# Kernel tuning notes

Hardware: AMD Instinct MI355X
Metric: run time of the kernel (lower is better)

Reference implementation:

```python
import jax, jax.numpy as jnp
import numpy as np

EPS = 1e-5        # torch BatchNorm2d default eps
G = 8             # DCNv4 groups
KP = 9            # 3x3 kernel points


def conv2d(x, w):
    return jax.lax.conv_general_dilated(
        x, w, window_strides=(1, 1), padding='SAME',
        dimension_numbers=('NCHW', 'OIHW', 'NCHW'))


def bn_eval(x, g_, b_, m_, v_):
    s = g_ / jnp.sqrt(v_ + EPS)
    return x * s[None, :, None, None] + (b_ - m_ * s)[None, :, None, None]


def silu(x):
    return x * jax.nn.sigmoid(x)


def dcnv4_core(value, offset, mask):
    # value: (N,H,W,G,Cg)  offset: (N,H,W,G,K,2) (x,y)  mask: (N,H,W,G,K) unnormalized (DCNv4: no softmax)
    N, H, W, Gn, Cg = value.shape
    r = jnp.arange(-1, 2, dtype=value.dtype)              # dilation=1, pad=1, 3x3 grid
    gy, gx = jnp.meshgrid(r, r, indexing='ij')
    grid_x = gx.ravel()  # (9,)
    grid_y = gy.ravel()
    px = jnp.arange(W, dtype=value.dtype)[None, None, :, None, None] + grid_x + offset[..., 0]
    py = jnp.arange(H, dtype=value.dtype)[None, :, None, None, None] + grid_y + offset[..., 1]
    x0 = jnp.floor(px); y0 = jnp.floor(py)
    lx = px - x0; ly = py - y0
    x0i = x0.astype(jnp.int32); y0i = y0.astype(jnp.int32)
    bidx = jnp.arange(N)[:, None, None, None, None]
    gidx = jnp.arange(Gn)[None, None, None, :, None]

    def tap(yi, xi, wgt):
        valid = (yi >= 0) & (yi < H) & (xi >= 0) & (xi < W)   # zero padding outside
        v = value[bidx, jnp.clip(yi, 0, H - 1), jnp.clip(xi, 0, W - 1), gidx]  # (N,H,W,G,K,Cg)
        return v * (wgt * valid)[..., None]

    s = (tap(y0i, x0i, (1 - ly) * (1 - lx))
         + tap(y0i, x0i + 1, (1 - ly) * lx)
         + tap(y0i + 1, x0i, ly * (1 - lx))
         + tap(y0i + 1, x0i + 1, ly * lx))
    return jnp.einsum('nhwgkc,nhwgk->nhwgc', s, mask)


def dcnv4(x, val_w, val_b, om_w, om_b, outp_w, outp_b):
    # x: NCHW. DCNv4 wrapper: flatten to tokens, value_proj, offset_mask linear on raw tokens,
    # deformable aggregation, output_proj, back to NCHW.
    N, C, H, W = x.shape
    t = x.transpose(0, 2, 3, 1).reshape(N, H * W, C)
    value = (t @ val_w.T + val_b).reshape(N, H, W, G, C // G)
    om = (t @ om_w.T + om_b).reshape(N, H, W, G, KP * 3)  # per group: 2K offsets then K masks
    offset = om[..., :2 * KP].reshape(N, H, W, G, KP, 2)
    mask = om[..., 2 * KP:]
    out = dcnv4_core(value, offset, mask).reshape(N, H * W, C)
    out = out @ outp_w.T + outp_b
    return out.reshape(N, H, W, C).transpose(0, 3, 1, 2)


def setup_inputs() -> dict:
    key = jax.random.key(0)
    ks = jax.random.split(key, 32)
    W_SC = 0.05
    d = {}
    d['x'] = jax.random.normal(ks[0], (4, 256, 64, 64), jnp.float32)
    d['cv1_w'] = jax.random.normal(ks[1], (128, 256, 3, 3), jnp.float32) * W_SC
    d['cv1_bn_g'] = jax.random.uniform(ks[2], (128,), jnp.float32, 0.5, 1.5)
    d['cv1_bn_b'] = jax.random.normal(ks[3], (128,), jnp.float32) * 0.1
    d['cv1_bn_m'] = jax.random.normal(ks[4], (128,), jnp.float32) * 0.1
    d['cv1_bn_v'] = jax.random.uniform(ks[5], (128,), jnp.float32, 0.5, 1.5)
    d['cv2_w'] = jax.random.normal(ks[6], (256, 128, 3, 3), jnp.float32) * W_SC
    d['cv2_bn_g'] = jax.random.uniform(ks[7], (256,), jnp.float32, 0.5, 1.5)
    d['cv2_bn_b'] = jax.random.normal(ks[8], (256,), jnp.float32) * 0.1
    d['cv2_bn_m'] = jax.random.normal(ks[9], (256,), jnp.float32) * 0.1
    d['cv2_bn_v'] = jax.random.uniform(ks[10], (256,), jnp.float32, 0.5, 1.5)
    d['val_w'] = jax.random.normal(ks[11], (256, 256), jnp.float32) * W_SC
    d['val_b'] = jax.random.normal(ks[12], (256,), jnp.float32) * 0.01
    d['om_w'] = jax.random.normal(ks[13], (216, 256), jnp.float32) * 0.02
    d['om_b'] = jax.random.normal(ks[14], (216,), jnp.float32) * 0.01
    d['outp_w'] = jax.random.normal(ks[15], (256, 256), jnp.float32) * W_SC
    d['outp_b'] = jax.random.normal(ks[16], (256,), jnp.float32) * 0.01
    d['bn3_g'] = jax.random.uniform(ks[17], (256,), jnp.float32, 0.5, 1.5)
    d['bn3_b'] = jax.random.normal(ks[18], (256,), jnp.float32) * 0.1
    d['bn3_m'] = jax.random.normal(ks[19], (256,), jnp.float32) * 0.1
    d['bn3_v'] = jax.random.uniform(ks[20], (256,), jnp.float32, 0.5, 1.5)
    d['pw1_w'] = jax.random.normal(ks[21], (768, 256, 1, 1), jnp.float32) * W_SC
    d['pw1_b'] = jax.random.normal(ks[22], (768,), jnp.float32) * 0.01
    d['pw2_w'] = jax.random.normal(ks[23], (256, 768, 1, 1), jnp.float32) * W_SC
    d['pw2_b'] = jax.random.normal(ks[24], (256,), jnp.float32) * 0.01
    return d


def reference(x, cv1_w, cv1_bn_g, cv1_bn_b, cv1_bn_m, cv1_bn_v,
              cv2_w, cv2_bn_g, cv2_bn_b, cv2_bn_m, cv2_bn_v,
              val_w, val_b, om_w, om_b, outp_w, outp_b,
              bn3_g, bn3_b, bn3_m, bn3_v, pw1_w, pw1_b, pw2_w, pw2_b):
    # cv2(cv1(x)) branch: Conv = Conv2d(no bias) + BN + SiLU
    y = silu(bn_eval(conv2d(x, cv1_w), cv1_bn_g, cv1_bn_b, cv1_bn_m, cv1_bn_v))
    y = silu(bn_eval(conv2d(y, cv2_w), cv2_bn_g, cv2_bn_b, cv2_bn_m, cv2_bn_v))
    # dcn branch: DCNv4 -> BN -> 1x1 conv (+SiLU) -> 1x1 conv
    d = dcnv4(x, val_w, val_b, om_w, om_b, outp_w, outp_b)
    d = bn_eval(d, bn3_g, bn3_b, bn3_m, bn3_v)
    d = silu(conv2d(d, pw1_w) + pw1_b[None, :, None, None])
    d = conv2d(d, pw2_w) + pw2_b[None, :, None, None]
    return x + y + d
```

## Files before the change

### kernel.cpp

```cpp
#include <hip/hip_runtime.h>
#include <math.h>

typedef __attribute__((ext_vector_type(8))) __bf16 bf16x8;
typedef __attribute__((ext_vector_type(8))) unsigned short us8;
typedef __attribute__((ext_vector_type(4))) unsigned short us4;
typedef __attribute__((ext_vector_type(4))) float f32x4;
typedef __attribute__((ext_vector_type(4))) int i32x4;
typedef unsigned int uint32;

#define EPSV 1e-5f

__device__ __forceinline__ float silu_f(float v) { return v / (1.f + __expf(-v)); }

__device__ __forceinline__ unsigned short f2bf(float f) {
  uint32 u = __builtin_bit_cast(uint32, f);
  u += 0x7fffu + ((u >> 16) & 1u);
  return (unsigned short)(u >> 16);
}
__device__ __forceinline__ float bf2f(unsigned short h) {
  uint32 u = ((uint32)h) << 16;
  return __builtin_bit_cast(float, u);
}

__device__ __forceinline__ void gl_lds16(const void* g, void* l) {
  __builtin_amdgcn_global_load_lds(
      (const __attribute__((address_space(1))) unsigned int*)g,
      (__attribute__((address_space(3))) unsigned int*)l, 16, 0, 0);
}

template <int EPI, int CIN, int BN>
__device__ __forceinline__ void gemm_body(
    int rb, int cb, int k0, int KL,
    const unsigned short* __restrict__ A, const unsigned short* __restrict__ Bw,
    const float* __restrict__ bias, int K, int Co, void* __restrict__ outv,
    const float* __restrict__ e0, const float* __restrict__ e1,
    const float* __restrict__ e2, const float* __restrict__ e3,
    const unsigned short* __restrict__ zpage, bf16x8* smem) {
  constexpr int NFR = BN / 32;
  constexpr int NB = BN / 64;
  constexpr int CPB = 512 + BN * 4;
  const int t = threadIdx.x;
  const int lane = t & 63;
  const int wv = t >> 6;
  const int wr = wv >> 1, wc = wv & 1;

  f32x4 acc[4][NFR];
#pragma unroll
  for (int i = 0; i < 4; i++)
#pragma unroll
    for (int j = 0; j < NFR; j++) acc[i][j] = (f32x4){0.f, 0.f, 0.f, 0.f};

  const unsigned short* Abase[2];
  int aprow[2], apcol[2], akoff[2];
#pragma unroll
  for (int i = 0; i < 2; i++) {
    int c = t + 256 * i;
    int row = (c >> 6) * 16 + (c & 15);
    int koff = ((c >> 4) & 3) * 8;
    akoff[i] = koff;
    int grow = rb + row;
    if constexpr (CIN > 0) {
      int n = grow >> 12, p = grow & 4095;
      aprow[i] = p >> 6;
      apcol[i] = p & 63;
      Abase[i] = A + (size_t)n * 4096 * CIN;
    } else {
      Abase[i] = A + (size_t)grow * K + koff;
    }
  }
  const unsigned short* Bbase[NB];
#pragma unroll
  for (int i = 0; i < NB; i++) {
    int c = t + 256 * i;
    int col = cb + (c >> 6) * 16 + (c & 15);
    int koff = ((c >> 4) & 3) * 8;
    Bbase[i] = (col < Co) ? (Bw + (size_t)col * K + koff) : zpage;
  }
  auto addrA = [&](int i, int kb) -> const unsigned short* {
    if constexpr (CIN > 0) {
      int tap = kb / CIN;
      int ci = (kb & (CIN - 1)) + akoff[i];
      int dy = tap / 3 - 1, dx = tap % 3 - 1;
      int h = aprow[i] + dy, w = apcol[i] + dx;
      if (((unsigned)h < 64u) & ((unsigned)w < 64u))
        return &Abase[i][(size_t)(h * 64 + w) * CIN + ci];
      return zpage;
    } else {
      return Abase[i] + kb;
    }
  };
  auto stage = [&](int buf, int kb) {
    bf16x8* base = &smem[buf * CPB];
    gl_lds16(addrA(0, kb), (void*)&base[t]);
    gl_lds16(addrA(1, kb), (void*)&base[t + 256]);
    gl_lds16((Bbase[0] == zpage) ? zpage : Bbase[0] + kb, (void*)&base[512 + t]);
    if constexpr (NB == 2)
      gl_lds16((Bbase[1] == zpage) ? zpage : Bbase[1] + kb,
               (void*)&base[512 + t + 256]);
  };

  const int nt = KL >> 5;
  stage(0, k0);
  __syncthreads();
  int cur = 0;
  for (int it = 0; it < nt; ++it) {
    if (it + 1 < nt) stage(cur ^ 1, k0 + ((it + 1) << 5));
    const bf16x8* Ab = &smem[cur * CPB];
    const bf16x8* Bb = Ab + 512;
    bf16x8 af[4], bfr[NFR];
#pragma unroll
    for (int mi = 0; mi < 4; mi++) af[mi] = Ab[(wr * 4 + mi) * 64 + lane];
#pragma unroll
    for (int ni = 0; ni < NFR; ni++) bfr[ni] = Bb[(wc * NFR + ni) * 64 + lane];
    __builtin_amdgcn_s_setprio(1);
#pragma unroll
    for (int mi = 0; mi < 4; mi++)
#pragma unroll
      for (int ni = 0; ni < NFR; ni++)
        acc[mi][ni] = __builtin_amdgcn_mfma_f32_16x16x32_bf16(af[mi], bfr[ni],
                                                              acc[mi][ni], 0, 0, 0);
    __builtin_amdgcn_s_setprio(0);
    __syncthreads();
    cur ^= 1;
  }

  const int lr = lane & 15, kg4 = (lane >> 4) * 4;
#pragma unroll
  for (int mi = 0; mi < 4; mi++) {
#pragma unroll
    for (int ni = 0; ni < NFR; ni++) {
      int gcol = cb + wc * (BN / 2) + ni * 16 + lr;
      if (gcol >= Co) continue;
      float bval, s = 1.f, tt = 0.f;
      if (EPI == 2 || EPI == 7) bval = 0.f;
      else if (EPI == 5) bval = (gcol < 256) ? bias[gcol] : e0[gcol - 256];
      else bval = bias[gcol];
      if (EPI == 2 || EPI == 3) {
        s = e0[gcol] * rsqrtf(e3[gcol] + EPSV);
        tt = e1[gcol] - e2[gcol] * s;
      }
      if (EPI == 6) {
        int grow0 = rb + wr * 64 + mi * 16 + kg4;
        int n = grow0 >> 12, p0 = grow0 & 4095;
        size_t oix = ((size_t)(n * 256 + gcol)) * 4096 + p0;
        f32x4 xv = *(const f32x4*)&((const float*)e0)[oix];
        const unsigned short* y2p = (const unsigned short*)e1;
        f32x4 ov;
#pragma unroll
        for (int j = 0; j < 4; j++) {
          float y2 = bf2f(y2p[((size_t)(n * 4096 + p0 + j)) * 256 + gcol]);
          ov[j] = acc[mi][ni][j] + bval + xv[j] + y2;
        }
        *(f32x4*)&((float*)outv)[oix] = ov;
        continue;
      }
#pragma unroll
      for (int j = 0; j < 4; j++) {
        int grow = rb + wr * 64 + mi * 16 + kg4 + j;
        float v = acc[mi][ni][j] + bval;
        if (EPI == 2) v = silu_f(v * s + tt);
        if (EPI == 3) v = v * s + tt;
        if (EPI == 4) v = silu_f(v);
        if (EPI == 7) {
          ((float*)outv)[(size_t)grow * Co + gcol] = v;
        } else if (EPI == 5) {
          if (gcol < 256)
            ((unsigned short*)outv)[(size_t)grow * 256 + gcol] = f2bf(v);
          else
            ((float*)e1)[(size_t)grow * 216 + (gcol - 256)] = v;
        } else {
          ((unsigned short*)outv)[(size_t)grow * Co + gcol] = f2bf(v);
        }
      }
    }
  }
}

__device__ __forceinline__ void dcn_body(
    int bid, const unsigned short* __restrict__ value,
    const float* __restrict__ om, unsigned short* __restrict__ out,
    void* smemraw) {
  f32x4* wgt = (f32x4*)smemraw;
  i32x4* adr = (i32x4*)((char*)smemraw + 288 * 16);
  const int n = bid >> 10;
  const int p0 = (bid & 1023) * 4;
  const int t = threadIdx.x;

  for (int idx = t; idx < 288; idx += 256) {
    int pi = idx / 72;
    int gk = idx - pi * 72;
    int g = gk / 9, k = gk - g * 9;
    int p = p0 + pi;
    int h0 = p >> 6, w0 = p & 63;
    const float* omp = om + ((size_t)(n * 4096 + p)) * 216 + g * 27;
    float ox = omp[2 * k], oy = omp[2 * k + 1], mk = omp[18 + k];
    float px = (float)(w0 + (k % 3) - 1) + ox;
    float py = (float)(h0 + (k / 3) - 1) + oy;
    float x0f = floorf(px), y0f = floorf(py);
    float lx = px - x0f, ly = py - y0f;
    int x0 = (int)x0f, y0 = (int)y0f;
    int x1 = x0 + 1, y1 = y0 + 1;
    bool vx0 = (unsigned)x0 < 64u, vx1 = (unsigned)x1 < 64u;
    bool vy0 = (unsigned)y0 < 64u, vy1 = (unsigned)y1 < 64u;
    int cx0 = min(max(x0, 0), 63), cx1 = min(max(x1, 0), 63);
    int cy0 = min(max(y0, 0), 63), cy1 = min(max(y1, 0), 63);
    f32x4 w4;
    w4[0] = (1.f - ly) * (1.f - lx) * mk * (float)(vy0 && vx0);
    w4[1] = (1.f - ly) * lx * mk * (float)(vy0 && vx1);
    w4[2] = ly * (1.f - lx) * mk * (float)(vy1 && vx0);
    w4[3] = ly * lx * mk * (float)(vy1 && vx1);
    i32x4 a4;
    a4[0] = (cy0 * 64 + cx0) * 256;
    a4[1] = (cy0 * 64 + cx1) * 256;
    a4[2] = (cy1 * 64 + cx0) * 256;
    a4[3] = (cy1 * 64 + cx1) * 256;
    wgt[idx] = w4;
    adr[idx] = a4;
  }
  __syncthreads();

  const int pi = t >> 6;
  const int g = (t >> 3) & 7;
  const int l = t & 7;
  const int p = p0 + pi;
  const unsigned short* vb = value + ((size_t)n * 4096) * 256 + g * 32 + l * 4;
  const int bix = (pi * 8 + g) * 9;
  float a0 = 0.f, a1 = 0.f, a2 = 0.f, a3 = 0.f;
#pragma unroll
  for (int k = 0; k < 9; k++) {
    f32x4 wv = wgt[bix + k];
    i32x4 av = adr[bix + k];
    us4 q0 = *(const us4*)(vb + av[0]);
    us4 q1 = *(const us4*)(vb + av[1]);
    us4 q2 = *(const us4*)(vb + av[2]);
    us4 q3 = *(const us4*)(vb + av[3]);
    a0 += wv[0] * bf2f(q0[0]) + wv[1] * bf2f(q1[0]) + wv[2] * bf2f(q2[0]) + wv[3] * bf2f(q3[0]);
    a1 += wv[0] * bf2f(q0[1]) + wv[1] * bf2f(q1[1]) + wv[2] * bf2f(q2[1]) + wv[3] * bf2f(q3[1]);
    a2 += wv[0] * bf2f(q0[2]) + wv[1] * bf2f(q1[2]) + wv[2] * bf2f(q2[2]) + wv[3] * bf2f(q3[2]);
    a3 += wv[0] * bf2f(q0[3]) + wv[1] * bf2f(q1[3]) + wv[2] * bf2f(q2[3]) + wv[3] * bf2f(q3[3]);
  }
  us4 o;
  o[0] = f2bf(a0); o[1] = f2bf(a1); o[2] = f2bf(a2); o[3] = f2bf(a3);
  *(us4*)&out[((size_t)(n * 4096 + p)) * 256 + g * 32 + l * 4] = o;
}

__global__ __launch_bounds__(256) void prep_k(
    const float* __restrict__ x, unsigned short* __restrict__ xt,
    const float* __restrict__ c1, unsigned short* __restrict__ o1,
    const float* __restrict__ c2, unsigned short* __restrict__ o2,
    const float* __restrict__ a0, unsigned short* __restrict__ b0,
    const float* __restrict__ a1, unsigned short* __restrict__ b1,
    const float* __restrict__ a2, unsigned short* __restrict__ b2,
    const float* __restrict__ a3, unsigned short* __restrict__ b3,
    const float* __restrict__ a4, unsigned short* __restrict__ b4,
    uint32* __restrict__ zp) {
  __shared__ float lds[64][65];
  int b = blockIdx.x;
  const int t = threadIdx.x;
  if (b == 0 && t < 32) zp[t] = 0u;
  if (b < 1024) {
    const int p0 = (b & 63) * 64, c0 = ((b >> 6) & 3) * 64, n = b >> 8;
    const int pp = t & 63, ccb = t >> 6;
    const float* xb = x + ((size_t)n * 256 + c0) * 4096 + p0;
#pragma unroll
    for (int i = 0; i < 16; i++) {
      int cc = ccb * 16 + i;
      lds[pp][cc] = xb[(size_t)cc * 4096 + pp];
    }
    __syncthreads();
#pragma unroll
    for (int i = 0; i < 2; i++) {
      int pp2 = (t >> 3) + i * 32;
      int c8 = (t & 7) * 8;
      us8 v;
#pragma unroll
      for (int j = 0; j < 8; j++) v[j] = f2bf(lds[pp2][c8 + j]);
      *(us8*)&xt[((size_t)(n * 4096 + p0 + pp2)) * 256 + c0 + c8] = v;
    }
    return;
  }
  int idx = (b - 1024) * 256 + t;
  if (idx < 294912) {
    int ci = idx & 255, r = idx >> 8;
    int tap = r % 9, co = r / 9;
    o1[idx] = f2bf(c1[((size_t)co * 256 + ci) * 9 + tap]);
    return;
  }
  idx -= 294912;
  if (idx < 294912) {
    int ci = idx & 127, r = idx >> 7;
    int tap = r % 9, co = r / 9;
    o2[idx] = f2bf(c2[((size_t)co * 128 + ci) * 9 + tap]);
    return;
  }
  idx -= 294912;
  const float* s;
  unsigned short* d;
  int off;
  if (idx < 65536)       { s = a0; d = b0; off = idx; }
  else if (idx < 120832) { s = a1; d = b1; off = idx - 65536; }
  else if (idx < 186368) { s = a2; d = b2; off = idx - 120832; }
  else if (idx < 382976) { s = a3; d = b3; off = idx - 186368; }
  else if (idx < 579584) { s = a4; d = b4; off = idx - 382976; }
  else return;
  d[off] = f2bf(s[off]);
}

__global__ __launch_bounds__(256) void fused_s1(
    const unsigned short* __restrict__ xt,
    const unsigned short* __restrict__ wc1, float* __restrict__ part,
    const unsigned short* __restrict__ wval, const float* __restrict__ val_b,
    const float* __restrict__ om_b, float* __restrict__ omf,
    unsigned short* __restrict__ valt, const unsigned short* __restrict__ zpage) {
  __shared__ bf16x8 smem[2048];
  int b = blockIdx.x;
  if (b < 512) {
    int s = b >> 7, mt = b & 127;
    gemm_body<7, 256, 128>(mt * 128, 0, s * 576, 576, xt, wc1, nullptr, 2304,
                           128, part + (size_t)s * 2097152, nullptr, nullptr,
                           nullptr, nullptr, zpage, smem);
  } else {
    b -= 512;
    gemm_body<5, 0, 128>((b >> 2) * 128, (b & 3) * 128, 0, 256, xt, wval, val_b,
                         256, 472, valt, om_b, (const float*)omf, nullptr,
                         nullptr, zpage, smem);
  }
}

__global__ __launch_bounds__(256) void fused_r(
    const float* __restrict__ part, const float* __restrict__ g1,
    const float* __restrict__ bb1, const float* __restrict__ m1,
    const float* __restrict__ v1, unsigned short* __restrict__ y1t,
    const unsigned short* __restrict__ valt, const float* __restrict__ omf,
    unsigned short* __restrict__ dcnt) {
  __shared__ char rsm[9216];
  int b = blockIdx.x;
  if (b < 1024) {
    int idx = b * 256 + threadIdx.x;
    int grow = idx >> 4;
    int co8 = (idx & 15) * 8;
    size_t base = (size_t)grow * 128 + co8;
    f32x4 s0 = *(const f32x4*)&part[base];
    f32x4 s1 = *(const f32x4*)&part[base + 4];
#pragma unroll
    for (int s = 1; s < 4; s++) {
      s0 += *(const f32x4*)&part[base + (size_t)s * 2097152];
      s1 += *(const f32x4*)&part[base + (size_t)s * 2097152 + 4];
    }
    us8 o;
#pragma unroll
    for (int j = 0; j < 8; j++) {
      int co = co8 + j;
      float sc = g1[co] * rsqrtf(v1[co] + EPSV);
      float tt = bb1[co] - m1[co] * sc;
      float v = (j < 4) ? s0[j] : s1[j - 4];
      o[j] = f2bf(silu_f(v * sc + tt));
    }
    *(us8*)&y1t[base] = o;
  } else {
    dcn_body(b - 1024, valt, omf, dcnt, (void*)rsm);
  }
}

__global__ __launch_bounds__(256) void fused_s2(
    const unsigned short* __restrict__ y1t,
    const unsigned short* __restrict__ wc2, const float* __restrict__ g2,
    const float* __restrict__ bb2, const float* __restrict__ m2,
    const float* __restrict__ v2, unsigned short* __restrict__ y2t,
    const unsigned short* __restrict__ dcnt, const unsigned short* __restrict__ woutp,
    const float* __restrict__ outp_b, const float* __restrict__ g3,
    const float* __restrict__ bb3, const float* __restrict__ m3,
    const float* __restrict__ v3, unsigned short* __restrict__ d1t,
    const unsigned short* __restrict__ zpage) {
  __shared__ bf16x8 smem[1536];
  int b = blockIdx.x;
  if (b < 512) {
    gemm_body<2, 128, 64>((b >> 2) * 128, (b & 3) * 64, 0, 1152, y1t, wc2,
                          nullptr, 1152, 256, y2t, g2, bb2, m2, v2, zpage, smem);
  } else {
    b -= 512;
    gemm_body<3, 0, 64>((b >> 2) * 128, (b & 3) * 64, 0, 256, dcnt, woutp,
                        outp_b, 256, 256, d1t, g3, bb3, m3, v3, zpage, smem);
  }
}

template <int EPI, int CIN, int BN>
__global__ __launch_bounds__(256) void gemm_k(
    const unsigned short* __restrict__ A, const unsigned short* __restrict__ Bw,
    const float* __restrict__ bias, int K, int Co, void* __restrict__ outv,
    const float* __restrict__ e0, const float* __restrict__ e1,
    const float* __restrict__ e2, const float* __restrict__ e3,
    const unsigned short* __restrict__ zpage) {
  __shared__ bf16x8 smem[2 * (512 + BN * 4)];
  gemm_body<EPI, CIN, BN>(blockIdx.y * 128, blockIdx.x * BN, 0, K, A, Bw, bias,
                          K, Co, outv, e0, e1, e2, e3, zpage, smem);
}

extern "C" void kernel_launch(void* const* d_in, const int* in_sizes, int n_in,
                              void* d_out, int out_size, void* d_ws,
                              size_t ws_size, hipStream_t stream) {
  const float* x      = (const float*)d_in[0];
  const float* cv1_w  = (const float*)d_in[1];
  const float* cv1_g  = (const float*)d_in[2];
  const float* cv1_b  = (const float*)d_in[3];
  const float* cv1_m  = (const float*)d_in[4];
  const float* cv1_v  = (const float*)d_in[5];
  const float* cv2_w  = (const float*)d_in[6];
  const float* cv2_g  = (const float*)d_in[7];
  const float* cv2_b  = (const float*)d_in[8];
  const float* cv2_m  = (const float*)d_in[9];
  const float* cv2_v  = (const float*)d_in[10];
  const float* val_w  = (const float*)d_in[11];
  const float* val_b  = (const float*)d_in[12];
  const float* om_w   = (const float*)d_in[13];
  const float* om_b   = (const float*)d_in[14];
  const float* outp_w = (const float*)d_in[15];
  const float* outp_b = (const float*)d_in[16];
  const float* bn3_g  = (const float*)d_in[17];
  const float* bn3_b  = (const float*)d_in[18];
  const float* bn3_m  = (const float*)d_in[19];
  const float* bn3_v  = (const float*)d_in[20];
  const float* pw1_w  = (const float*)d_in[21];
  const float* pw1_b  = (const float*)d_in[22];
  const float* pw2_w  = (const float*)d_in[23];
  const float* pw2_b  = (const float*)d_in[24];
  float* out = (float*)d_out;

  char* w = (char*)d_ws;
  auto alloc = [&](size_t bytes) {
    char* p = w;
    w += (bytes + 255) & ~(size_t)255;
    return p;
  };
  unsigned short* xt    = (unsigned short*)alloc(16384ull * 256 * 2);
  unsigned short* y1t   = (unsigned short*)alloc(16384ull * 128 * 2);
  unsigned short* y2t   = (unsigned short*)alloc(16384ull * 256 * 2);
  unsigned short* valt  = (unsigned short*)alloc(16384ull * 256 * 2);
  float*          omf   = (float*)alloc(16384ull * 216 * 4);
  unsigned short* dcnt  = (unsigned short*)alloc(16384ull * 256 * 2);
  unsigned short* d1t   = (unsigned short*)alloc(16384ull * 256 * 2);
  unsigned short* p1t   = (unsigned short*)alloc(16384ull * 768 * 2);
  float* part = (float*)d1t;
  unsigned short* wc1   = (unsigned short*)alloc(128ull * 2304 * 2);
  unsigned short* wc2   = (unsigned short*)alloc(256ull * 1152 * 2);
  unsigned short* wval  = (unsigned short*)alloc(256ull * 256 * 2);
  unsigned short* wom   = (unsigned short*)alloc(216ull * 256 * 2);
  unsigned short* woutp = (unsigned short*)alloc(256ull * 256 * 2);
  unsigned short* wpw1  = (unsigned short*)alloc(768ull * 256 * 2);
  unsigned short* wpw2  = (unsigned short*)alloc(256ull * 768 * 2);
  unsigned short* zpage = (unsigned short*)alloc(256);

  prep_k<<<5592, 256, 0, stream>>>(x, xt, cv1_w, wc1, cv2_w, wc2, val_w, wval,
                                   om_w, wom, outp_w, woutp, pw1_w, wpw1,
                                   pw2_w, wpw2, (uint32*)zpage);

  fused_s1<<<1024, 256, 0, stream>>>(xt, wc1, part, wval, val_b, om_b, omf,
                                     valt, zpage);

  fused_r<<<5120, 256, 0, stream>>>(part, cv1_g, cv1_b, cv1_m, cv1_v, y1t,
                                    valt, omf, dcnt);

  fused_s2<<<1024, 256, 0, stream>>>(y1t, wc2, cv2_g, cv2_b, cv2_m, cv2_v, y2t,
                                     dcnt, woutp, outp_b, bn3_g, bn3_b, bn3_m,
                                     bn3_v, d1t, zpage);

  gemm_k<4, 0, 128><<<dim3(6, 128), 256, 0, stream>>>(
      d1t, wpw1, pw1_b, 256, 768, p1t, nullptr, nullptr, nullptr, nullptr, zpage);
  gemm_k<6, 0, 64><<<dim3(4, 128), 256, 0, stream>>>(
      p1t, wpw2, pw2_b, 768, 256, out, x, (const float*)y2t, nullptr, nullptr, zpage);
}
```

Measured before the change: 164.7 us.

## Swizzle blocks across XCDs, store split-K partials as bf16, restructure weight prep

Adds an XCD-aware block index swizzle to every fused and GEMM kernel, so neighbouring logical tiles land on the same XCD's L2 and heterogeneous work (conv vs value GEMM, reduce vs DCN) is interleaved. The split-K conv1 partials are now written and read as bf16 instead of fp32 (EPI 7 falls through to the bf16 store), halving that traffic at some accuracy cost from rounding the partial sums. The conv weight repack has each thread read 9 contiguous taps, shrinking the prep grid.

```diff
diff --git a/kernel.cpp b/kernel.cpp
--- a/kernel.cpp
+++ b/kernel.cpp
@@ -20,6 +20,10 @@
 __device__ __forceinline__ float bf2f(unsigned short h) {
   uint32 u = ((uint32)h) << 16;
   return __builtin_bit_cast(float, u);
+}
+
+__device__ __forceinline__ int xswz(int b, int n) {
+  return (b & 7) * (n >> 3) + (b >> 3);
 }
 
 __device__ __forceinline__ void gl_lds16(const void* g, void* l) {
@@ -161,9 +165,7 @@
         if (EPI == 2) v = silu_f(v * s + tt);
         if (EPI == 3) v = v * s + tt;
         if (EPI == 4) v = silu_f(v);
-        if (EPI == 7) {
-          ((float*)outv)[(size_t)grow * Co + gcol] = v;
-        } else if (EPI == 5) {
+        if (EPI == 5) {
           if (gcol < 256)
             ((unsigned short*)outv)[(size_t)grow * 256 + gcol] = f2bf(v);
           else
@@ -279,21 +281,25 @@
     }
     return;
   }
-  int idx = (b - 1024) * 256 + t;
-  if (idx < 294912) {
-    int ci = idx & 255, r = idx >> 8;
-    int tap = r % 9, co = r / 9;
-    o1[idx] = f2bf(c1[((size_t)co * 256 + ci) * 9 + tap]);
+  if (b < 1152) {
+    int idx = (b - 1024) * 256 + t;
+    int co = idx >> 8, ci = idx & 255;
+    const float* src = c1 + (size_t)(co * 256 + ci) * 9;
+#pragma unroll
+    for (int tap = 0; tap < 9; tap++)
+      o1[(size_t)(co * 9 + tap) * 256 + ci] = f2bf(src[tap]);
     return;
   }
-  idx -= 294912;
-  if (idx < 294912) {
-    int ci = idx & 127, r = idx >> 7;
-    int tap = r % 9, co = r / 9;
-    o2[idx] = f2bf(c2[((size_t)co * 128 + ci) * 9 + tap]);
+  if (b < 1280) {
+    int idx = (b - 1152) * 256 + t;
+    int co = idx >> 7, ci = idx & 127;
+    const float* src = c2 + (size_t)(co * 128 + ci) * 9;
+#pragma unroll
+    for (int tap = 0; tap < 9; tap++)
+      o2[(size_t)(co * 9 + tap) * 128 + ci] = f2bf(src[tap]);
     return;
   }
-  idx -= 294912;
+  int idx = (b - 1280) * 256 + t;
   const float* s;
   unsigned short* d;
   int off;
@@ -308,44 +314,46 @@
 
 __global__ __launch_bounds__(256) void fused_s1(
     const unsigned short* __restrict__ xt,
-    const unsigned short* __restrict__ wc1, float* __restrict__ part,
+    const unsigned short* __restrict__ wc1, unsigned short* __restrict__ part,
     const unsigned short* __restrict__ wval, const float* __restrict__ val_b,
     const float* __restrict__ om_b, float* __restrict__ omf,
     unsigned short* __restrict__ valt, const unsigned short* __restrict__ zpage) {
   __shared__ bf16x8 smem[2048];
-  int b = blockIdx.x;
-  if (b < 512) {
-    int s = b >> 7, mt = b & 127;
+  int l = xswz(blockIdx.x, 1024);
+  if ((l & 1) == 0) {
+    int c = l >> 1;
+    int s = c >> 7, mt = c & 127;
     gemm_body<7, 256, 128>(mt * 128, 0, s * 576, 576, xt, wc1, nullptr, 2304,
                            128, part + (size_t)s * 2097152, nullptr, nullptr,
                            nullptr, nullptr, zpage, smem);
   } else {
-    b -= 512;
-    gemm_body<5, 0, 128>((b >> 2) * 128, (b & 3) * 128, 0, 256, xt, wval, val_b,
+    int v = l >> 1;
+    gemm_body<5, 0, 128>((v >> 2) * 128, (v & 3) * 128, 0, 256, xt, wval, val_b,
                          256, 472, valt, om_b, (const float*)omf, nullptr,
                          nullptr, zpage, smem);
   }
 }
 
 __global__ __launch_bounds__(256) void fused_r(
-    const float* __restrict__ part, const float* __restrict__ g1,
+    const unsigned short* __restrict__ part, const float* __restrict__ g1,
     const float* __restrict__ bb1, const float* __restrict__ m1,
     const float* __restrict__ v1, unsigned short* __restrict__ y1t,
     const unsigned short* __restrict__ valt, const float* __restrict__ omf,
     unsigned short* __restrict__ dcnt) {
   __shared__ char rsm[9216];
-  int b = blockIdx.x;
-  if (b < 1024) {
-    int idx = b * 256 + threadIdx.x;
-    int grow = idx >> 4;
-    int co8 = (idx & 15) * 8;
+  int l = xswz(blockIdx.x, 5120);
+  int q = l / 5, r5 = l - q * 5;
+  if (r5 == 0) {
+    int g = q * 256 + threadIdx.x;
+    int grow = g >> 4;
+    int co8 = (g & 15) << 3;
     size_t base = (size_t)grow * 128 + co8;
-    f32x4 s0 = *(const f32x4*)&part[base];
-    f32x4 s1 = *(const f32x4*)&part[base + 4];
-#pragma unroll
-    for (int s = 1; s < 4; s++) {
-      s0 += *(const f32x4*)&part[base + (size_t)s * 2097152];
-      s1 += *(const f32x4*)&part[base + (size_t)s * 2097152 + 4];
+    float sum[8] = {0.f, 0.f, 0.f, 0.f, 0.f, 0.f, 0.f, 0.f};
+#pragma unroll
+    for (int s = 0; s < 4; s++) {
+      us8 pv = *(const us8*)&part[base + (size_t)s * 2097152];
+#pragma unroll
+      for (int j = 0; j < 8; j++) sum[j] += bf2f(pv[j]);
     }
     us8 o;
 #pragma unroll
@@ -353,12 +361,11 @@
       int co = co8 + j;
       float sc = g1[co] * rsqrtf(v1[co] + EPSV);
       float tt = bb1[co] - m1[co] * sc;
-      float v = (j < 4) ? s0[j] : s1[j - 4];
-      o[j] = f2bf(silu_f(v * sc + tt));
+      o[j] = f2bf(silu_f(sum[j] * sc + tt));
     }
     *(us8*)&y1t[base] = o;
   } else {
-    dcn_body(b - 1024, valt, omf, dcnt, (void*)rsm);
+    dcn_body(q * 4 + r5 - 1, valt, omf, dcnt, (void*)rsm);
   }
 }
 
@@ -373,18 +380,19 @@
     const float* __restrict__ v3, unsigned short* __restrict__ d1t,
     const unsigned short* __restrict__ zpage) {
   __shared__ bf16x8 smem[1536];
-  int b = blockIdx.x;
-  if (b < 512) {
-    gemm_body<2, 128, 64>((b >> 2) * 128, (b & 3) * 64, 0, 1152, y1t, wc2,
+  int l = xswz(blockIdx.x, 1024);
+  if ((l & 1) == 0) {
+    int c = l >> 1;
+    gemm_body<2, 128, 64>((c >> 2) * 128, (c & 3) * 64, 0, 1152, y1t, wc2,
                           nullptr, 1152, 256, y2t, g2, bb2, m2, v2, zpage, smem);
   } else {
-    b -= 512;
-    gemm_body<3, 0, 64>((b >> 2) * 128, (b & 3) * 64, 0, 256, dcnt, woutp,
+    int v = l >> 1;
+    gemm_body<3, 0, 64>((v >> 2) * 128, (v & 3) * 64, 0, 256, dcnt, woutp,
                         outp_b, 256, 256, d1t, g3, bb3, m3, v3, zpage, smem);
   }
 }
 
-template <int EPI, int CIN, int BN>
+template <int EPI, int CIN, int BN, int NCB, int GRID>
 __global__ __launch_bounds__(256) void gemm_k(
     const unsigned short* __restrict__ A, const unsigned short* __restrict__ Bw,
     const float* __restrict__ bias, int K, int Co, void* __restrict__ outv,
@@ -392,7 +400,8 @@
     const float* __restrict__ e2, const float* __restrict__ e3,
     const unsigned short* __restrict__ zpage) {
   __shared__ bf16x8 smem[2 * (512 + BN * 4)];
-  gemm_body<EPI, CIN, BN>(blockIdx.y * 128, blockIdx.x * BN, 0, K, A, Bw, bias,
+  int l = xswz(blockIdx.x, GRID);
+  gemm_body<EPI, CIN, BN>((l / NCB) * 128, (l % NCB) * BN, 0, K, A, Bw, bias,
                           K, Co, outv, e0, e1, e2, e3, zpage, smem);
 }
 
@@ -440,7 +449,7 @@
   unsigned short* dcnt  = (unsigned short*)alloc(16384ull * 256 * 2);
   unsigned short* d1t   = (unsigned short*)alloc(16384ull * 256 * 2);
   unsigned short* p1t   = (unsigned short*)alloc(16384ull * 768 * 2);
-  float* part = (float*)d1t;
+  unsigned short* part = d1t;
   unsigned short* wc1   = (unsigned short*)alloc(128ull * 2304 * 2);
   unsigned short* wc2   = (unsigned short*)alloc(256ull * 1152 * 2);
   unsigned short* wval  = (unsigned short*)alloc(256ull * 256 * 2);
@@ -450,7 +459,7 @@
   unsigned short* wpw2  = (unsigned short*)alloc(256ull * 768 * 2);
   unsigned short* zpage = (unsigned short*)alloc(256);
 
-  prep_k<<<5592, 256, 0, stream>>>(x, xt, cv1_w, wc1, cv2_w, wc2, val_w, wval,
+  prep_k<<<3544, 256, 0, stream>>>(x, xt, cv1_w, wc1, cv2_w, wc2, val_w, wval,
                                    om_w, wom, outp_w, woutp, pw1_w, wpw1,
                                    pw2_w, wpw2, (uint32*)zpage);
 
@@ -464,8 +473,8 @@
                                      dcnt, woutp, outp_b, bn3_g, bn3_b, bn3_m,
                                      bn3_v, d1t, zpage);
 
-  gemm_k<4, 0, 128><<<dim3(6, 128), 256, 0, stream>>>(
+  gemm_k<4, 0, 128, 6, 768><<<768, 256, 0, stream>>>(
       d1t, wpw1, pw1_b, 256, 768, p1t, nullptr, nullptr, nullptr, nullptr, zpage);
-  gemm_k<6, 0, 64><<<dim3(4, 128), 256, 0, stream>>>(
+  gemm_k<6, 0, 64, 4, 512><<<512, 256, 0, stream>>>(
       p1t, wpw2, pw2_b, 768, 256, out, x, (const float*)y2t, nullptr, nullptr, zpage);
 }
```

New measurement: 176.6 us. +7.2%, slower.
